# Kernel optimization log

Hardware: AMD Instinct MI355X
Metric: run time of the kernel (lower is better)

## Reference

```python
import jax, jax.numpy as jnp
import numpy as np

NUM_NODES = 500000
EMB = 200        # embedding_size
U = 10           # embedding_u_size
T = 4            # edge_type_count
DIM_A = 20
N_SRC = 65536
N_DST = 8192
E = 262144       # edges per edge type


def setup_inputs() -> dict:
    key = jax.random.key(0)
    ks = jax.random.split(key, 9)
    std = 1.0 / np.sqrt(EMB)
    return {
        "input_nodes": jax.random.randint(ks[0], (N_SRC,), 0, NUM_NODES),
        "output_nodes": jax.random.randint(ks[1], (N_DST,), 0, NUM_NODES),
        "edge_src": jax.random.randint(ks[2], (T, E), 0, N_SRC),
        "edge_dst": jax.random.randint(ks[3], (T, E), 0, N_DST),
        "node_embeddings": jax.random.uniform(ks[4], (NUM_NODES, EMB), jnp.float32, -1.0, 1.0),
        "node_type_embeddings": jax.random.uniform(ks[5], (NUM_NODES, T, U), jnp.float32, -1.0, 1.0),
        "trans_weights": std * jax.random.normal(ks[6], (T, U, EMB), jnp.float32),
        "trans_weights_s1": std * jax.random.normal(ks[7], (T, U, DIM_A), jnp.float32),
        "trans_weights_s2": std * jax.random.normal(ks[8], (T, DIM_A, 1), jnp.float32),
    }


def reference(input_nodes, output_nodes, edge_src, edge_dst,
              node_embeddings, node_type_embeddings,
              trans_weights, trans_weights_s1, trans_weights_s2):
    n_dst = output_nodes.shape[0]
    # gather per-type embeddings of source nodes: [N_src, T, U] -> [T, N_src, U]
    src_feat = jnp.moveaxis(node_type_embeddings[input_nodes], 1, 0)
    # per-edge-type copy_u + sum (scatter-add over dst nodes): [T, N_dst, U]
    agg = jax.vmap(lambda es, ed, f: jax.ops.segment_sum(f[es], ed, num_segments=n_dst))(
        edge_src, edge_dst, src_feat)
    nte = jnp.moveaxis(agg, 0, 1)  # [B, T, U]
    # attention scores: tanh(nte @ s1_t) @ s2_t per (node, type)
    h = jnp.tanh(jnp.einsum('btu,tua->bta', nte, trans_weights_s1))      # [B, T, A]
    scores = jnp.einsum('bta,ta->bt', h, trans_weights_s2[..., 0])        # [B, T]
    att = jax.nn.softmax(scores, axis=1)                                  # [B, T]
    # attention-weighted combine (repeat in torch makes all T rows identical)
    combined = jnp.einsum('bt,btu->bu', att, nte)                         # [B, U]
    # final per-type projection + base embedding
    out = node_embeddings[output_nodes][:, None, :] + \
        jnp.einsum('bu,tue->bte', combined, trans_weights)                # [B, T, EMB]
    # F.normalize(dim=2), eps=1e-12
    norm = jnp.linalg.norm(out, axis=2, keepdims=True)
    return out / jnp.maximum(norm, 1e-12)
```

## Files before the change

kernel.cpp:

```cpp
#include <hip/hip_runtime.h>
#include <math.h>

#define T_CNT 4
#define U_DIM 10
#define A_DIM 20
#define EMB_D 200
#define N_SRC 65536
#define N_DST 8192
#define E_PER_T 262144

#define NCHUNK 8
#define DCHUNK (N_DST / NCHUNK)
#define NSEG_MAIN 32
#define ESEG_MAIN (E_PER_T / NSEG_MAIN)

__global__ __launch_bounds__(256)
void gather_kernel(const int* __restrict__ input_nodes,
                   const float4* __restrict__ nte4,
                   float4* __restrict__ src_feat4) {
    int id = blockIdx.x * 256 + threadIdx.x;
    if (id >= N_SRC * U_DIM) return;
    int i = id / 10;
    int q = id - i * 10;
    int node = input_nodes[i];
    src_feat4[i * 10 + q] = nte4[(size_t)node * 10 + q];
}

template <int ESEG>
__global__ __launch_bounds__(256)
void scan_kernel(const int* __restrict__ edge_src,
                 const int* __restrict__ edge_dst,
                 const float* __restrict__ src_feat,
                 float* __restrict__ part) {
    __shared__ float acc[DCHUNK * U_DIM];

    const int b = blockIdx.x;
    const int c = b & (NCHUNK - 1);
    const int t = (b >> 3) & (T_CNT - 1);
    const int s = b >> 5;
    const int base = c * DCHUNK;

    for (int i = threadIdx.x; i < DCHUNK * U_DIM; i += 256) acc[i] = 0.f;
    __syncthreads();

    const int* ed = edge_dst + (size_t)t * E_PER_T + (size_t)s * ESEG;
    const int* es = edge_src + (size_t)t * E_PER_T + (size_t)s * ESEG;

    constexpr int ITERS = ESEG / 1024;
    int k = threadIdx.x * 4;
    int4 d_cur = *reinterpret_cast<const int4*>(ed + k);
    int4 s_cur = *reinterpret_cast<const int4*>(es + k);

#pragma unroll
    for (int it = 0; it < ITERS; ++it) {
        int4 d_nxt = make_int4(0, 0, 0, 0), s_nxt = make_int4(0, 0, 0, 0);
        if (it + 1 < ITERS) {
            d_nxt = *reinterpret_cast<const int4*>(ed + k + 1024);
            s_nxt = *reinterpret_cast<const int4*>(es + k + 1024);
        }
        int dsts[4] = {d_cur.x, d_cur.y, d_cur.z, d_cur.w};
        int srcs[4] = {s_cur.x, s_cur.y, s_cur.z, s_cur.w};
        unsigned r[4];
        bool p[4];
#pragma unroll
        for (int j = 0; j < 4; ++j) {
            r[j] = (unsigned)(dsts[j] - base);
            p[j] = r[j] < DCHUNK;
        }
        float2 vals[4][5];
#pragma unroll
        for (int j = 0; j < 4; ++j) {
            if (p[j]) {
                const float2* f2 = reinterpret_cast<const float2*>(
                    src_feat + (size_t)srcs[j] * (T_CNT * U_DIM) + t * U_DIM);
#pragma unroll
                for (int q = 0; q < 5; ++q) vals[j][q] = f2[q];
            }
        }
#pragma unroll
        for (int j = 0; j < 4; ++j) {
            if (p[j]) {
                int off = (int)r[j] * U_DIM;
#pragma unroll
                for (int q = 0; q < 5; ++q) {
                    atomicAdd(&acc[off + 2 * q],     vals[j][q].x);
                    atomicAdd(&acc[off + 2 * q + 1], vals[j][q].y);
                }
            }
        }
        d_cur = d_nxt;
        s_cur = s_nxt;
        k += 1024;
    }
    __syncthreads();

    float* outp = part + (((size_t)(s * T_CNT + t)) * N_DST + base) * U_DIM;
    for (int i = threadIdx.x; i < DCHUNK * U_DIM; i += 256) outp[i] = acc[i];
}

__global__ __launch_bounds__(256)
void scan_kernel_gen(const int* __restrict__ edge_src,
                     const int* __restrict__ edge_dst,
                     const float* __restrict__ src_feat,
                     float* __restrict__ part, int eseg) {
    __shared__ float acc[DCHUNK * U_DIM];
    const int b = blockIdx.x;
    const int c = b & (NCHUNK - 1);
    const int t = (b >> 3) & (T_CNT - 1);
    const int s = b >> 5;
    const int base = c * DCHUNK;
    for (int i = threadIdx.x; i < DCHUNK * U_DIM; i += 256) acc[i] = 0.f;
    __syncthreads();
    const int* ed = edge_dst + (size_t)t * E_PER_T + (size_t)s * eseg;
    const int* es = edge_src + (size_t)t * E_PER_T + (size_t)s * eseg;
    for (int k = threadIdx.x * 4; k < eseg; k += 1024) {
        int4 d4 = *reinterpret_cast<const int4*>(ed + k);
        int4 s4 = *reinterpret_cast<const int4*>(es + k);
        int dsts[4] = {d4.x, d4.y, d4.z, d4.w};
        int srcs[4] = {s4.x, s4.y, s4.z, s4.w};
#pragma unroll
        for (int j = 0; j < 4; ++j) {
            unsigned r = (unsigned)(dsts[j] - base);
            if (r < DCHUNK) {
                const float2* f2 = reinterpret_cast<const float2*>(
                    src_feat + (size_t)srcs[j] * (T_CNT * U_DIM) + t * U_DIM);
                int off = (int)r * U_DIM;
#pragma unroll
                for (int q = 0; q < 5; ++q) {
                    float2 v = f2[q];
                    atomicAdd(&acc[off + 2 * q], v.x);
                    atomicAdd(&acc[off + 2 * q + 1], v.y);
                }
            }
        }
    }
    __syncthreads();
    float* outp = part + (((size_t)(s * T_CNT + t)) * N_DST + base) * U_DIM;
    for (int i = threadIdx.x; i < DCHUNK * U_DIM; i += 256) outp[i] = acc[i];
}

template <int NSEG>
__global__ __launch_bounds__(256)
void finalize_kernel(const float* __restrict__ part,
                     const int* __restrict__ output_nodes,
                     const float* __restrict__ node_emb,
                     const float* __restrict__ W,
                     const float* __restrict__ S1,
                     const float* __restrict__ S2,
                     float* __restrict__ out) {
    const int b = blockIdx.x;
    const int tid = threadIdx.x;

    __shared__ float sNte[T_CNT * U_DIM];
    __shared__ float sH[T_CNT * A_DIM];
    __shared__ float sScore[T_CNT];
    __shared__ float sAtt[T_CNT];
    __shared__ float sComb[U_DIM];
    __shared__ float sBase[EMB_D];

    if (tid < T_CNT * U_DIM) {
        const float* p = part + (size_t)b * U_DIM +
                         ((size_t)(tid / U_DIM) * N_DST) * U_DIM + (tid % U_DIM);
        float v[NSEG];
#pragma unroll
        for (int s = 0; s < NSEG; ++s)
            v[s] = p[(size_t)s * (T_CNT * N_DST * U_DIM)];
        float sum = 0.f;
#pragma unroll
        for (int s = 0; s < NSEG; ++s) sum += v[s];
        sNte[tid] = sum;
    }
    const int on = output_nodes[b];
    if (tid < EMB_D) sBase[tid] = node_emb[(size_t)on * EMB_D + tid];
    __syncthreads();

    if (tid < T_CNT * A_DIM) {
        int t = tid / A_DIM, a = tid - t * A_DIM;
        float s = 0.f;
#pragma unroll
        for (int u = 0; u < U_DIM; ++u)
            s += sNte[t * U_DIM + u] * S1[t * (U_DIM * A_DIM) + u * A_DIM + a];
        sH[tid] = tanhf(s);
    }
    __syncthreads();

    if (tid < T_CNT) {
        float s = 0.f;
#pragma unroll
        for (int a = 0; a < A_DIM; ++a)
            s += sH[tid * A_DIM + a] * S2[tid * A_DIM + a];
        sScore[tid] = s;
    }
    __syncthreads();

    if (tid == 0) {
        float m = sScore[0];
#pragma unroll
        for (int t = 1; t < T_CNT; ++t) m = fmaxf(m, sScore[t]);
        float sum = 0.f;
#pragma unroll
        for (int t = 0; t < T_CNT; ++t) {
            float e = __expf(sScore[t] - m);
            sAtt[t] = e;
            sum += e;
        }
        float inv = 1.f / sum;
#pragma unroll
        for (int t = 0; t < T_CNT; ++t) sAtt[t] *= inv;
    }
    __syncthreads();

    if (tid < U_DIM) {
        float s = 0.f;
#pragma unroll
        for (int t = 0; t < T_CNT; ++t) s += sAtt[t] * sNte[t * U_DIM + tid];
        sComb[tid] = s;
    }
    __syncthreads();

    const int t = tid >> 6;
    const int lane = tid & 63;
    float c[U_DIM];
#pragma unroll
    for (int u = 0; u < U_DIM; ++u) c[u] = sComb[u];

    float v[4];
    float sq = 0.f;
#pragma unroll
    for (int j = 0; j < 4; ++j) {
        int e = lane + j * 64;
        if (e < EMB_D) {
            float s = sBase[e];
            const float* w = W + t * (U_DIM * EMB_D) + e;
#pragma unroll
            for (int u = 0; u < U_DIM; ++u) s += c[u] * w[u * EMB_D];
            v[j] = s;
            sq += s * s;
        }
    }
#pragma unroll
    for (int off = 32; off > 0; off >>= 1) sq += __shfl_xor(sq, off);

    float n = sqrtf(sq);
    float inv = 1.f / fmaxf(n, 1e-12f);

    float* o = out + (size_t)b * (T_CNT * EMB_D) + t * EMB_D;
#pragma unroll
    for (int j = 0; j < 4; ++j) {
        int e = lane + j * 64;
        if (e < EMB_D) o[e] = v[j] * inv;
    }
}

extern "C" void kernel_launch(void* const* d_in, const int* in_sizes, int n_in,
                              void* d_out, int out_size, void* d_ws, size_t ws_size,
                              hipStream_t stream) {
    const int*   input_nodes   = (const int*)d_in[0];
    const int*   output_nodes  = (const int*)d_in[1];
    const int*   edge_src      = (const int*)d_in[2];
    const int*   edge_dst      = (const int*)d_in[3];
    const float* node_emb      = (const float*)d_in[4];
    const float* node_type_emb = (const float*)d_in[5];
    const float* W             = (const float*)d_in[6];
    const float* S1            = (const float*)d_in[7];
    const float* S2            = (const float*)d_in[8];
    float*       out           = (float*)d_out;

    const size_t gatherBytes = (size_t)N_SRC * T_CNT * U_DIM * sizeof(float);
    const size_t segBytes = (size_t)T_CNT * N_DST * U_DIM * sizeof(float);
    const size_t needMain = gatherBytes + NSEG_MAIN * segBytes;

    float* src_feat = (float*)d_ws;

    if (ws_size >= needMain) {
        float* part = (float*)((char*)d_ws + gatherBytes);
        const int n = N_SRC * U_DIM;
        gather_kernel<<<(n + 255) / 256, 256, 0, stream>>>(
            input_nodes, (const float4*)node_type_emb, (float4*)src_feat);
        scan_kernel<ESEG_MAIN><<<NCHUNK * T_CNT * NSEG_MAIN, 256, 0, stream>>>(
            edge_src, edge_dst, src_feat, part);
        finalize_kernel<NSEG_MAIN><<<N_DST, 256, 0, stream>>>(
            part, output_nodes, node_emb, W, S1, S2, out);
    } else {
        bool pre = ws_size >= gatherBytes + segBytes;
        size_t avail = pre ? (ws_size - gatherBytes) : ws_size;
        int nseg = (int)(avail / segBytes);
        if (nseg > NSEG_MAIN) nseg = NSEG_MAIN;
        if (nseg < 1) nseg = 1;
        while (nseg & (nseg - 1)) nseg--;
        const int eseg = E_PER_T / nseg;
        float* part = pre ? (float*)((char*)d_ws + gatherBytes) : (float*)d_ws;
        const float* feat = node_type_emb;
        if (pre) {
            const int n = N_SRC * U_DIM;
            gather_kernel<<<(n + 255) / 256, 256, 0, stream>>>(
                input_nodes, (const float4*)node_type_emb, (float4*)src_feat);
            feat = src_feat;
        }
        scan_kernel_gen<<<NCHUNK * T_CNT * nseg, 256, 0, stream>>>(
            edge_src, edge_dst, feat, part, eseg);
        switch (nseg) {
            case 32: finalize_kernel<32><<<N_DST, 256, 0, stream>>>(part, output_nodes, node_emb, W, S1, S2, out); break;
            case 16: finalize_kernel<16><<<N_DST, 256, 0, stream>>>(part, output_nodes, node_emb, W, S1, S2, out); break;
            case 8:  finalize_kernel<8><<<N_DST, 256, 0, stream>>>(part, output_nodes, node_emb, W, S1, S2, out); break;
            case 4:  finalize_kernel<4><<<N_DST, 256, 0, stream>>>(part, output_nodes, node_emb, W, S1, S2, out); break;
            case 2:  finalize_kernel<2><<<N_DST, 256, 0, stream>>>(part, output_nodes, node_emb, W, S1, S2, out); break;
            default: finalize_kernel<1><<<N_DST, 256, 0, stream>>>(part, output_nodes, node_emb, W, S1, S2, out); break;
        }
    }
}
```

Before: 582.4 us.

## Pad gathered source features to 12-float stride and use 1024-thread scan blocks

The gather kernel now writes each node's per-type 10-float feature into a 12-float padded slot, so the scan kernel can load it with two float4 loads and one float2 load instead of five float2 loads. The main scan kernel switches to 1024-thread blocks and cuts the number of edge segments from 32 to 8. That shrinks the partial-sum buffer that finalize must reduce and lowers launch count, but gives each block fewer, larger segments. Padding raises gather storage by 20%. The fallback path always gathers now, which may break with very small workspaces.

```diff
diff --git a/kernel.cpp b/kernel.cpp
--- a/kernel.cpp
+++ b/kernel.cpp
@@ -11,23 +11,32 @@
 
 #define NCHUNK 8
 #define DCHUNK (N_DST / NCHUNK)
-#define NSEG_MAIN 32
+
+#define SF_TSTRIDE 12
+#define SF_STRIDE (T_CNT * SF_TSTRIDE)
+
+#define NSEG_MAIN 8
 #define ESEG_MAIN (E_PER_T / NSEG_MAIN)
 
 __global__ __launch_bounds__(256)
 void gather_kernel(const int* __restrict__ input_nodes,
-                   const float4* __restrict__ nte4,
-                   float4* __restrict__ src_feat4) {
+                   const float2* __restrict__ nte2,
+                   float* __restrict__ sf) {
     int id = blockIdx.x * 256 + threadIdx.x;
-    if (id >= N_SRC * U_DIM) return;
-    int i = id / 10;
-    int q = id - i * 10;
+    if (id >= N_SRC * T_CNT) return;
+    int i = id >> 2;
+    int t = id & 3;
     int node = input_nodes[i];
-    src_feat4[i * 10 + q] = nte4[(size_t)node * 10 + q];
+    const float2* src = nte2 + ((size_t)node * (T_CNT * U_DIM) + t * U_DIM) / 2;
+    float2 v0 = src[0], v1 = src[1], v2 = src[2], v3 = src[3], v4 = src[4];
+    float* dst = sf + (size_t)id * SF_TSTRIDE;
+    *reinterpret_cast<float4*>(dst)     = make_float4(v0.x, v0.y, v1.x, v1.y);
+    *reinterpret_cast<float4*>(dst + 4) = make_float4(v2.x, v2.y, v3.x, v3.y);
+    *reinterpret_cast<float2*>(dst + 8) = v4;
 }
 
 template <int ESEG>
-__global__ __launch_bounds__(256)
+__global__ __launch_bounds__(1024)
 void scan_kernel(const int* __restrict__ edge_src,
                  const int* __restrict__ edge_dst,
                  const float* __restrict__ src_feat,
@@ -40,13 +49,13 @@
     const int s = b >> 5;
     const int base = c * DCHUNK;
 
-    for (int i = threadIdx.x; i < DCHUNK * U_DIM; i += 256) acc[i] = 0.f;
+    for (int i = threadIdx.x; i < DCHUNK * U_DIM; i += 1024) acc[i] = 0.f;
     __syncthreads();
 
     const int* ed = edge_dst + (size_t)t * E_PER_T + (size_t)s * ESEG;
     const int* es = edge_src + (size_t)t * E_PER_T + (size_t)s * ESEG;
 
-    constexpr int ITERS = ESEG / 1024;
+    constexpr int ITERS = ESEG / 4096;
     int k = threadIdx.x * 4;
     int4 d_cur = *reinterpret_cast<const int4*>(ed + k);
     int4 s_cur = *reinterpret_cast<const int4*>(es + k);
@@ -55,8 +64,8 @@
     for (int it = 0; it < ITERS; ++it) {
         int4 d_nxt = make_int4(0, 0, 0, 0), s_nxt = make_int4(0, 0, 0, 0);
         if (it + 1 < ITERS) {
-            d_nxt = *reinterpret_cast<const int4*>(ed + k + 1024);
-            s_nxt = *reinterpret_cast<const int4*>(es + k + 1024);
+            d_nxt = *reinterpret_cast<const int4*>(ed + k + 4096);
+            s_nxt = *reinterpret_cast<const int4*>(es + k + 4096);
         }
         int dsts[4] = {d_cur.x, d_cur.y, d_cur.z, d_cur.w};
         int srcs[4] = {s_cur.x, s_cur.y, s_cur.z, s_cur.w};
@@ -67,35 +76,41 @@
             r[j] = (unsigned)(dsts[j] - base);
             p[j] = r[j] < DCHUNK;
         }
-        float2 vals[4][5];
+        float4 va[4], vb[4];
+        float2 vc[4];
 #pragma unroll
         for (int j = 0; j < 4; ++j) {
             if (p[j]) {
-                const float2* f2 = reinterpret_cast<const float2*>(
-                    src_feat + (size_t)srcs[j] * (T_CNT * U_DIM) + t * U_DIM);
-#pragma unroll
-                for (int q = 0; q < 5; ++q) vals[j][q] = f2[q];
+                const float* fp = src_feat + (size_t)srcs[j] * SF_STRIDE + t * SF_TSTRIDE;
+                va[j] = *reinterpret_cast<const float4*>(fp);
+                vb[j] = *reinterpret_cast<const float4*>(fp + 4);
+                vc[j] = *reinterpret_cast<const float2*>(fp + 8);
             }
         }
 #pragma unroll
         for (int j = 0; j < 4; ++j) {
             if (p[j]) {
-                int off = (int)r[j] * U_DIM;
-#pragma unroll
-                for (int q = 0; q < 5; ++q) {
-                    atomicAdd(&acc[off + 2 * q],     vals[j][q].x);
-                    atomicAdd(&acc[off + 2 * q + 1], vals[j][q].y);
-                }
+                float* a = acc + (int)r[j] * U_DIM;
+                atomicAdd(a + 0, va[j].x);
+                atomicAdd(a + 1, va[j].y);
+                atomicAdd(a + 2, va[j].z);
+                atomicAdd(a + 3, va[j].w);
+                atomicAdd(a + 4, vb[j].x);
+                atomicAdd(a + 5, vb[j].y);
+                atomicAdd(a + 6, vb[j].z);
+                atomicAdd(a + 7, vb[j].w);
+                atomicAdd(a + 8, vc[j].x);
+                atomicAdd(a + 9, vc[j].y);
             }
         }
         d_cur = d_nxt;
         s_cur = s_nxt;
-        k += 1024;
+        k += 4096;
     }
     __syncthreads();
 
     float* outp = part + (((size_t)(s * T_CNT + t)) * N_DST + base) * U_DIM;
-    for (int i = threadIdx.x; i < DCHUNK * U_DIM; i += 256) outp[i] = acc[i];
+    for (int i = threadIdx.x; i < DCHUNK * U_DIM; i += 1024) outp[i] = acc[i];
 }
 
 __global__ __launch_bounds__(256)
@@ -122,15 +137,16 @@
         for (int j = 0; j < 4; ++j) {
             unsigned r = (unsigned)(dsts[j] - base);
             if (r < DCHUNK) {
-                const float2* f2 = reinterpret_cast<const float2*>(
-                    src_feat + (size_t)srcs[j] * (T_CNT * U_DIM) + t * U_DIM);
-                int off = (int)r * U_DIM;
-#pragma unroll
-                for (int q = 0; q < 5; ++q) {
-                    float2 v = f2[q];
-                    atomicAdd(&acc[off + 2 * q], v.x);
-                    atomicAdd(&acc[off + 2 * q + 1], v.y);
-                }
+                const float* fp = src_feat + (size_t)srcs[j] * SF_STRIDE + t * SF_TSTRIDE;
+                float4 va = *reinterpret_cast<const float4*>(fp);
+                float4 vb = *reinterpret_cast<const float4*>(fp + 4);
+                float2 vc = *reinterpret_cast<const float2*>(fp + 8);
+                float* a = acc + (int)r * U_DIM;
+                atomicAdd(a + 0, va.x); atomicAdd(a + 1, va.y);
+                atomicAdd(a + 2, va.z); atomicAdd(a + 3, va.w);
+                atomicAdd(a + 4, vb.x); atomicAdd(a + 5, vb.y);
+                atomicAdd(a + 6, vb.z); atomicAdd(a + 7, vb.w);
+                atomicAdd(a + 8, vc.x); atomicAdd(a + 9, vc.y);
             }
         }
     }
@@ -266,39 +282,34 @@
     const float* S2            = (const float*)d_in[8];
     float*       out           = (float*)d_out;
 
-    const size_t gatherBytes = (size_t)N_SRC * T_CNT * U_DIM * sizeof(float);
+    const size_t gatherBytes = (size_t)N_SRC * SF_STRIDE * sizeof(float);
     const size_t segBytes = (size_t)T_CNT * N_DST * U_DIM * sizeof(float);
     const size_t needMain = gatherBytes + NSEG_MAIN * segBytes;
 
     float* src_feat = (float*)d_ws;
 
+    const int nGather = N_SRC * T_CNT;
+
     if (ws_size >= needMain) {
         float* part = (float*)((char*)d_ws + gatherBytes);
-        const int n = N_SRC * U_DIM;
-        gather_kernel<<<(n + 255) / 256, 256, 0, stream>>>(
-            input_nodes, (const float4*)node_type_emb, (float4*)src_feat);
-        scan_kernel<ESEG_MAIN><<<NCHUNK * T_CNT * NSEG_MAIN, 256, 0, stream>>>(
+        gather_kernel<<<(nGather + 255) / 256, 256, 0, stream>>>(
+            input_nodes, (const float2*)node_type_emb, src_feat);
+        scan_kernel<ESEG_MAIN><<<NCHUNK * T_CNT * NSEG_MAIN, 1024, 0, stream>>>(
             edge_src, edge_dst, src_feat, part);
         finalize_kernel<NSEG_MAIN><<<N_DST, 256, 0, stream>>>(
             part, output_nodes, node_emb, W, S1, S2, out);
     } else {
-        bool pre = ws_size >= gatherBytes + segBytes;
-        size_t avail = pre ? (ws_size - gatherBytes) : ws_size;
+        size_t avail = (ws_size > gatherBytes) ? (ws_size - gatherBytes) : 0;
         int nseg = (int)(avail / segBytes);
-        if (nseg > NSEG_MAIN) nseg = NSEG_MAIN;
+        if (nseg > 32) nseg = 32;
         if (nseg < 1) nseg = 1;
         while (nseg & (nseg - 1)) nseg--;
         const int eseg = E_PER_T / nseg;
-        float* part = pre ? (float*)((char*)d_ws + gatherBytes) : (float*)d_ws;
-        const float* feat = node_type_emb;
-        if (pre) {
-            const int n = N_SRC * U_DIM;
-            gather_kernel<<<(n + 255) / 256, 256, 0, stream>>>(
-                input_nodes, (const float4*)node_type_emb, (float4*)src_feat);
-            feat = src_feat;
-        }
+        float* part = (float*)((char*)d_ws + gatherBytes);
+        gather_kernel<<<(nGather + 255) / 256, 256, 0, stream>>>(
+            input_nodes, (const float2*)node_type_emb, src_feat);
         scan_kernel_gen<<<NCHUNK * T_CNT * nseg, 256, 0, stream>>>(
-            edge_src, edge_dst, feat, part, eseg);
+            edge_src, edge_dst, src_feat, part, eseg);
         switch (nseg) {
             case 32: finalize_kernel<32><<<N_DST, 256, 0, stream>>>(part, output_nodes, node_emb, W, S1, S2, out); break;
             case 16: finalize_kernel<16><<<N_DST, 256, 0, stream>>>(part, output_nodes, node_emb, W, S1, S2, out); break;
```

Result: no change. 574.5 us (-1.4%).
